# Optimization experiments

Hardware: AMD Instinct MI355X
Metric: run time of the kernel (lower is better)

## Reference

```python
import jax, jax.numpy as jnp
import numpy as np

N, E, D, G, L = 100_000, 500_000, 128, 512, 4
BN_EPS = 1e-5

def _bn(v, g, b):
    # BatchNorm1d in training mode: biased batch stats over node/graph axis
    m = v.mean(0)
    var = v.var(0)
    return (v - m) * jax.lax.rsqrt(var + BN_EPS) * g + b

def setup_inputs() -> dict:
    key = jax.random.key(0)
    ks = jax.random.split(key, 12)
    s = 0.05
    return {
        "x": jax.random.normal(ks[0], (N, D), jnp.float32),
        "edge_index": jax.random.randint(ks[1], (2, E), 0, N, jnp.int64),
        "batch": jnp.sort(jax.random.randint(ks[2], (N,), 0, G, jnp.int64)),
        "num_graphs": G,
        "W1": jax.random.normal(ks[3], (L, D, 2 * D), jnp.float32) * s,
        "b1": jnp.zeros((L, 2 * D), jnp.float32),
        "g1": jnp.ones((L, 2 * D), jnp.float32),
        "be1": jnp.zeros((L, 2 * D), jnp.float32),
        "W2": jax.random.normal(ks[4], (L, 2 * D, D), jnp.float32) * s,
        "b2": jnp.zeros((L, D), jnp.float32),
        "gbn": jnp.ones((L, D), jnp.float32),
        "bbn": jnp.zeros((L, D), jnp.float32),
        "eps": jnp.zeros((L,), jnp.float32),
        "cW1": jax.random.normal(ks[5], (3 * D, D), jnp.float32) * s,
        "cb1": jnp.zeros((D,), jnp.float32),
        "cg": jnp.ones((D,), jnp.float32),
        "cbeta": jnp.zeros((D,), jnp.float32),
        "cW2": jax.random.normal(ks[6], (D, D // 2), jnp.float32) * s,
        "cb2": jnp.zeros((D // 2,), jnp.float32),
        "cW3": jax.random.normal(ks[7], (D // 2, 2), jnp.float32) * s,
        "cb3": jnp.zeros((2,), jnp.float32),
    }

def reference(x, edge_index, batch, num_graphs, W1, b1, g1, be1, W2, b2, gbn, bbn, eps,
              cW1, cb1, cg, cbeta, cW2, cb2, cW3, cb3):
    n = x.shape[0]
    src, dst = edge_index[0], edge_index[1]
    for l in range(W1.shape[0]):
        # GINConv: mlp((1+eps)*x + sum_{j in N(i)} x_j)  (scatter-add to dst)
        agg = jax.ops.segment_sum(x[src], dst, num_segments=n)
        h = (1.0 + eps[l]) * x + agg
        h = jax.nn.relu(_bn(h @ W1[l] + b1[l], g1[l], be1[l]))
        h = h @ W2[l] + b2[l]
        x = jax.nn.relu(_bn(h, gbn[l], bbn[l]))  # outer BN + ReLU (dropout off: eval)
    # multi-pool readout: add / mean / max per graph
    s = jax.ops.segment_sum(x, batch, num_segments=num_graphs)
    cnt = jax.ops.segment_sum(jnp.ones((n,), x.dtype), batch, num_segments=num_graphs)
    mean = s / jnp.maximum(cnt, 1.0)[:, None]
    mx = jax.ops.segment_max(x, batch, num_segments=num_graphs)
    z = jnp.concatenate([s, mean, mx], axis=-1)  # [G, 3*D]
    z = jax.nn.relu(_bn(z @ cW1 + cb1, cg, cbeta))
    z = jax.nn.relu(z @ cW2 + cb2)
    return z @ cW3 + cb3
```

## Files before the change

### kernel.cpp

```cpp
#include <hip/hip_runtime.h>
#include <cstdint>
#include <cstddef>

#define NN 100000
#define EE 500000
#define DD 128
#define GG 512
#define LL 4
#define BN_EPS 1e-5f

typedef __attribute__((ext_vector_type(8))) short short8;
typedef __attribute__((ext_vector_type(8))) unsigned short ushort8v;
typedef __attribute__((ext_vector_type(4))) float f32x4;

static __device__ __forceinline__ unsigned short f2bf(float f) {
  union { float f; unsigned u; } v;
  v.f = f;
  unsigned r = v.u + 0x7fffu + ((v.u >> 16) & 1u);
  return (unsigned short)(r >> 16);
}
static __device__ __forceinline__ float bf2f(unsigned short u) {
  union { unsigned u; float f; } v;
  v.u = ((unsigned)u) << 16;
  return v.f;
}


__global__ void k_hist(const int* __restrict__ ei, int* __restrict__ cnt) {
  int e = blockIdx.x * 256 + threadIdx.x;
  if (e < EE) {
    int d = ei[EE + e];
    if (d >= 0 && d < NN) atomicAdd(&cnt[d], 1);
  }
}

__global__ void k_part(const int* __restrict__ cnt, int* __restrict__ part) {
  __shared__ int sm[1024];
  int t = threadIdx.x;
  int i = blockIdx.x * 1024 + t;
  sm[t] = (i < NN) ? cnt[i] : 0;
  __syncthreads();
  for (int off = 512; off > 0; off >>= 1) {
    if (t < off) sm[t] += sm[t + off];
    __syncthreads();
  }
  if (t == 0) part[blockIdx.x] = sm[0];
}

__global__ void k_scanpart(const int* __restrict__ part, int* __restrict__ partx, int nb) {
  __shared__ int sm[128];
  int t = threadIdx.x;
  int v = (t < nb) ? part[t] : 0;
  sm[t] = v;
  __syncthreads();
  for (int off = 1; off < 128; off <<= 1) {
    int u = (t >= off) ? sm[t - off] : 0;
    __syncthreads();
    sm[t] += u;
    __syncthreads();
  }
  if (t < nb) partx[t] = sm[t] - v;
}

__global__ void k_rs(const int* __restrict__ cnt, const int* __restrict__ partx,
                     int* __restrict__ rs, int* __restrict__ cur) {
  __shared__ int sm[1024];
  int t = threadIdx.x;
  int i = blockIdx.x * 1024 + t;
  int v = (i < NN) ? cnt[i] : 0;
  sm[t] = v;
  __syncthreads();
  for (int off = 1; off < 1024; off <<= 1) {
    int u = (t >= off) ? sm[t - off] : 0;
    __syncthreads();
    sm[t] += u;
    __syncthreads();
  }
  if (i < NN) {
    int excl = partx[blockIdx.x] + sm[t] - v;
    rs[i] = excl;
    cur[i] = excl;
    if (i == NN - 1) rs[NN] = excl + v;
  }
}

__global__ void k_fill(const int* __restrict__ ei, int* __restrict__ cur,
                       int* __restrict__ ci) {
  int e = blockIdx.x * 256 + threadIdx.x;
  if (e < EE) {
    int s = ei[e];
    int d = ei[EE + e];
    if (d >= 0 && d < NN && s >= 0 && s < NN) {
      int pos = atomicAdd(&cur[d], 1);
      if (pos >= 0 && pos < EE) ci[pos] = s;
    }
  }
}


__global__ void k_conv(const float* __restrict__ W1, const float* __restrict__ W2,
                       unsigned short* __restrict__ W1t, unsigned short* __restrict__ W2t) {
  int idx = blockIdx.x * 256 + threadIdx.x;
  if (idx < 4 * 256 * 128) {
    {
      int l = idx >> 15, rem = idx & 32767;
      int nc = rem >> 7, k = rem & 127;
      W1t[idx] = f2bf(W1[(l << 15) + k * 256 + nc]);
    }
    {
      int l = idx >> 15, rem = idx & 32767;
      int nc = rem >> 8, k = rem & 255;
      W2t[idx] = f2bf(W2[(l << 15) + k * 128 + nc]);
    }
  }
}


__global__ void k_x2bf(const float* __restrict__ x, unsigned short* __restrict__ xb) {
  int i = blockIdx.x * 256 + threadIdx.x;
  if (i < NN * DD / 4) {
    float4 v = *(const float4*)(x + (size_t)i * 4);
    ushort4 o;
    o.x = f2bf(v.x); o.y = f2bf(v.y); o.z = f2bf(v.z); o.w = f2bf(v.w);
    *(ushort4*)(xb + (size_t)i * 4) = o;
  }
}


__global__ __launch_bounds__(256) void k_agg_bf16(
    const unsigned short* __restrict__ X, const int* __restrict__ rs,
    const int* __restrict__ ci, const float* __restrict__ epsv, int l, int mode,
    const float* __restrict__ tsc, const float* __restrict__ tsh,
    unsigned short* __restrict__ h0, int n) {
  int idx = blockIdx.x * 256 + threadIdx.x;
  int node = idx >> 4;
  int c8 = (idx & 15) << 3;
  if (node >= n) return;
  float sa[8], sb[8];
  if (mode) {
    float4 a0 = *(const float4*)(tsc + c8), a1 = *(const float4*)(tsc + c8 + 4);
    float4 b0 = *(const float4*)(tsh + c8), b1 = *(const float4*)(tsh + c8 + 4);
    sa[0] = a0.x; sa[1] = a0.y; sa[2] = a0.z; sa[3] = a0.w;
    sa[4] = a1.x; sa[5] = a1.y; sa[6] = a1.z; sa[7] = a1.w;
    sb[0] = b0.x; sb[1] = b0.y; sb[2] = b0.z; sb[3] = b0.w;
    sb[4] = b1.x; sb[5] = b1.y; sb[6] = b1.z; sb[7] = b1.w;
  }
  float se = 1.f + epsv[l];
  ushort8v v = *(const ushort8v*)(X + (size_t)node * DD + c8);
  float acc[8];
#pragma unroll
  for (int j = 0; j < 8; ++j) {
    float f = bf2f(v[j]);
    if (mode) f = fmaxf(0.f, f * sa[j] + sb[j]);
    acc[j] = se * f;
  }
  int e0 = rs[node], e1 = rs[node + 1];
  ushort8v un;
  if (e0 < e1) un = *(const ushort8v*)(X + (size_t)ci[e0] * DD + c8);
  for (int e = e0; e < e1; ++e) {
    ushort8v uc = un;
    if (e + 1 < e1) un = *(const ushort8v*)(X + (size_t)ci[e + 1] * DD + c8);
#pragma unroll
    for (int j = 0; j < 8; ++j) {
      float f = bf2f(uc[j]);
      if (mode) f = fmaxf(0.f, f * sa[j] + sb[j]);
      acc[j] += f;
    }
  }
  ushort8v o;
#pragma unroll
  for (int j = 0; j < 8; ++j) o[j] = f2bf(acc[j]);
  *(ushort8v*)(h0 + (size_t)node * DD + c8) = o;
}


__global__ __launch_bounds__(512) void k_mom(
    const unsigned short* __restrict__ h0, float* __restrict__ M2s,
    float* __restrict__ css, int n) {
  constexpr int HT = 264;
  constexpr int NCH = (NN + 255) / 256;
  constexpr int NBLK = 196;
  __shared__ __align__(16) unsigned short Ht[128 * HT];
  __shared__ float lcs[128];
  int tid = threadIdx.x;
  int lane = tid & 63, wave = tid >> 6;
  int quad = lane >> 4, l15 = lane & 15;
  if (tid < 128) lcs[tid] = 0.f;
  int c8 = (tid & 15) << 3;
  int rloc = tid >> 4;
  float csr[8];
#pragma unroll
  for (int j = 0; j < 8; ++j) csr[j] = 0.f;
  f32x4 acc[8];
#pragma unroll
  for (int j = 0; j < 8; ++j) acc[j] = (f32x4){0.f, 0.f, 0.f, 0.f};

  for (int ch = blockIdx.x; ch < NCH; ch += NBLK) {
    int n0 = ch * 256;
    __syncthreads();
#pragma unroll
    for (int pass = 0; pass < 8; ++pass) {
      int nl = rloc + pass * 32;
      int gr = n0 + nl;
      ushort8v v = (ushort8v){0, 0, 0, 0, 0, 0, 0, 0};
      if (gr < n) v = *(const ushort8v*)(h0 + (size_t)gr * DD + c8);
#pragma unroll
      for (int j = 0; j < 8; ++j) {
        int row = c8 + j;
        int sb = (nl >> 3) ^ ((row >> 3) & 7);
        Ht[row * HT + (sb << 3) + (nl & 7)] = v[j];
        csr[j] += bf2f(v[j]);
      }
    }
    __syncthreads();
#pragma unroll
    for (int kc = 0; kc < 8; ++kc) {
      int b = kc * 4 + quad;
      int arow = wave * 16 + l15;
      short8 avv =
          *(const short8*)(&Ht[arow * HT + ((b ^ ((arow >> 3) & 7)) << 3)]);
#pragma unroll
      for (int j = 0; j < 8; ++j) {
        int brow = j * 16 + l15;
        short8 bvv =
            *(const short8*)(&Ht[brow * HT + ((b ^ ((brow >> 3) & 7)) << 3)]);
        acc[j] = __builtin_amdgcn_mfma_f32_16x16x32_bf16(avv, bvv, acc[j], 0, 0, 0);
      }
    }
  }
  float* M2 = M2s + (size_t)blockIdx.x * 16384;
  int lr = wave * 16 + quad * 4;
#pragma unroll
  for (int j = 0; j < 8; ++j)
#pragma unroll
    for (int g = 0; g < 4; ++g)
      M2[(lr + g) * 128 + j * 16 + l15] = acc[j][g];
#pragma unroll
  for (int j = 0; j < 8; ++j) atomicAdd(&lcs[c8 + j], csr[j]);
  __syncthreads();
  if (tid < 128) css[(size_t)blockIdx.x * 128 + tid] = lcs[tid];
}

__global__ void k_red(const float* __restrict__ M2s, const float* __restrict__ css,
                      float* __restrict__ M2f, float* __restrict__ csf) {
  int i = blockIdx.x * 256 + threadIdx.x;
  float s = 0.f;
  for (int k = 0; k < 196; ++k) s += M2s[(size_t)k * 16384 + i];
  M2f[i] = s;
  if (i < 128) {
    float c = 0.f;
    for (int k = 0; k < 196; ++k) c += css[(size_t)k * 128 + i];
    csf[i] = c;
  }
}

__global__ __launch_bounds__(128) void k_bn1(
    const float* __restrict__ M2, const float* __restrict__ cs,
    const unsigned short* __restrict__ W1t_l, const float* __restrict__ g1_l,
    const float* __restrict__ be1_l, float* __restrict__ osc,
    float* __restrict__ osh) {
  __shared__ float wsh[128];
  __shared__ float red1[2], red2[2];
  int c = blockIdx.x, t = threadIdx.x;
  float w = bf2f(W1t_l[c * 128 + t]);
  wsh[t] = w;
  __syncthreads();
  float inner = 0.f;
#pragma unroll 4
  for (int k = 0; k < 128; ++k) inner = fmaf(M2[t * 128 + k], wsh[k], inner);
  float s1 = w * inner;
  float s2 = w * cs[t];
#pragma unroll
  for (int off = 32; off > 0; off >>= 1) {
    s1 += __shfl_xor(s1, off, 64);
    s2 += __shfl_xor(s2, off, 64);
  }
  if ((t & 63) == 0) { red1[t >> 6] = s1; red2[t >> 6] = s2; }
  __syncthreads();
  if (t == 0) {
    float q = (red1[0] + red1[1]) * (1.0f / NN);
    float um = (red2[0] + red2[1]) * (1.0f / NN);
    float var = fmaxf(q - um * um, 0.f);
    float sc = g1_l[c] * rsqrtf(var + BN_EPS);
    osc[c] = sc;
    osh[c] = be1_l[c] - um * sc;
  }
}


__global__ __launch_bounds__(512, 4) void k_gfused(
    const unsigned short* __restrict__ A, const float* __restrict__ sc1,
    const float* __restrict__ sh1, const unsigned short* __restrict__ W1t_l,
    const unsigned short* __restrict__ W2t_l, const float* __restrict__ b2_l,
    unsigned short* __restrict__ C, float* __restrict__ psum,
    float* __restrict__ psq, int n) {
  constexpr int BST = 72;
  constexpr int HP = 136;
  __shared__ __align__(16) unsigned short Bsm[2][128 * BST];
  __shared__ __align__(16) unsigned short H[128 * HP];
  __shared__ float bsum[128], bsq[128];

  int tid = threadIdx.x;
  int lane = tid & 63, wave = tid >> 6;
  int quad = lane >> 4, l15 = lane & 15;
  int row0 = blockIdx.x * 128;
  int r = row0 + wave * 16 + l15;
  bool valid = r < n;

  short8 av[4];
#pragma unroll
  for (int ks = 0; ks < 4; ++ks) {
    av[ks] = (short8){0, 0, 0, 0, 0, 0, 0, 0};
    if (valid) av[ks] = *(const short8*)(A + (size_t)r * 128 + ks * 32 + quad * 8);
  }

  ushort8v pA[2], pB[2];
  f32x4 acc1[8], acc2[8];
#pragma unroll
  for (int j = 0; j < 8; ++j) acc1[j] = (f32x4){0.f, 0.f, 0.f, 0.f};
#pragma unroll
  for (int j = 0; j < 8; ++j) acc2[j] = (f32x4){0.f, 0.f, 0.f, 0.f};

#define LD_W1(dst, cg, kc)                                                      \
  {                                                                             \
    _Pragma("unroll") for (int it = 0; it < 2; ++it) {                          \
      int f = tid + it * 512, rr = f >> 3, cc = (f & 7) << 3;                   \
      dst[it] = *(const ushort8v*)(W1t_l + (size_t)((cg)*128 + rr) * 128 +      \
                                   (kc)*64 + cc);                               \
    }                                                                           \
  }
#define LD_W2(dst, kc2)                                                         \
  {                                                                             \
    _Pragma("unroll") for (int it = 0; it < 2; ++it) {                          \
      int f = tid + it * 512, rr = f >> 3, cc = (f & 7) << 3;                   \
      dst[it] = *(const ushort8v*)(W2t_l + (size_t)rr * 256 + (kc2)*64 + cc);   \
    }                                                                           \
  }
#define ST_B(buf, src)                                                          \
  {                                                                             \
    _Pragma("unroll") for (int it = 0; it < 2; ++it) {                          \
      int f = tid + it * 512, rr = f >> 3, cc = (f & 7) << 3;                   \
      *(ushort8v*)(&Bsm[buf][rr * BST + cc]) = src[it];                         \
    }                                                                           \
  }
#define MM1(buf, k2)                                                            \
  {                                                                             \
    _Pragma("unroll") for (int kk = 0; kk < 2; ++kk) {                          \
      int ko = kk * 32 + quad * 8;                                              \
      short8 a = av[(k2)*2 + kk];                                               \
      _Pragma("unroll") for (int cf = 0; cf < 8; ++cf) {                        \
        short8 bv = *(const short8*)(&Bsm[buf][(cf * 16 + l15) * BST + ko]);    \
        acc1[cf] = __builtin_amdgcn_mfma_f32_16x16x32_bf16(a, bv, acc1[cf],     \
                                                           0, 0, 0);            \
      }                                                                         \
    }                                                                           \
  }
#define MM2(buf, half)                                                          \
  {                                                                             \
    _Pragma("unroll") for (int kk = 0; kk < 64; kk += 32) {                     \
      int ko = kk + quad * 8;                                                   \
      short8 a = *(const short8*)(&H[(wave * 16 + l15) * HP + (half)*64 + ko]); \
      _Pragma("unroll") for (int cf = 0; cf < 8; ++cf) {                        \
        short8 bv = *(const short8*)(&Bsm[buf][(cf * 16 + l15) * BST + ko]);    \
        acc2[cf] = __builtin_amdgcn_mfma_f32_16x16x32_bf16(a, bv, acc2[cf],     \
                                                           0, 0, 0);            \
      }                                                                         \
    }                                                                           \
  }
#define EPI(cg)                                                                 \
  {                                                                             \
    int lrb = wave * 16 + quad * 4;                                             \
    _Pragma("unroll") for (int cf = 0; cf < 8; ++cf) {                          \
      int col = (cg)*128 + cf * 16 + l15;                                       \
      float sc = sc1[col], sh = sh1[col];                                       \
      _Pragma("unroll") for (int g = 0; g < 4; ++g)                             \
          H[(lrb + g) * HP + cf * 16 + l15] =                                   \
              f2bf(fmaxf(0.f, acc1[cf][g] * sc + sh));                          \
    }                                                                           \
  }
#define ZACC1                                                                   \
  {                                                                             \
    _Pragma("unroll") for (int j = 0; j < 8; ++j)                               \
        acc1[j] = (f32x4){0.f, 0.f, 0.f, 0.f};                                  \
  }

  LD_W1(pA, 0, 0)
  LD_W1(pB, 0, 1)
  ST_B(0, pA)
  __syncthreads();
  LD_W2(pA, 0) MM1(0, 0) ST_B(1, pB) __syncthreads();
  LD_W2(pB, 1) MM1(1, 1) EPI(0) ST_B(0, pA) __syncthreads();
  LD_W1(pA, 1, 0) MM2(0, 0) ST_B(1, pB) __syncthreads();
  LD_W1(pB, 1, 1) MM2(1, 1) ST_B(0, pA) __syncthreads();
  LD_W2(pA, 2) ZACC1 MM1(0, 0) ST_B(1, pB) __syncthreads();
  LD_W2(pB, 3) MM1(1, 1) EPI(1) ST_B(0, pA) __syncthreads();
  MM2(0, 0) ST_B(1, pB) __syncthreads();
  MM2(1, 1)

  __syncthreads();
  unsigned short* Ct = H;
  if (tid < 128) { bsum[tid] = 0.f; bsq[tid] = 0.f; }
  float s8[8], q8[8];
#pragma unroll
  for (int j = 0; j < 8; ++j) { s8[j] = 0.f; q8[j] = 0.f; }
  int lrbase = wave * 16 + quad * 4;
#pragma unroll
  for (int cf = 0; cf < 8; ++cf) {
    float bv = b2_l[cf * 16 + l15];
#pragma unroll
    for (int g = 0; g < 4; ++g) {
      int lr = lrbase + g;
      float e = acc2[cf][g] + bv;
      Ct[lr * HP + cf * 16 + l15] = f2bf(e);
      if (row0 + lr < n) { s8[cf] += e; q8[cf] += e * e; }
    }
  }
#pragma unroll
  for (int cf = 0; cf < 8; ++cf) {
    s8[cf] += __shfl_xor(s8[cf], 16, 64);
    s8[cf] += __shfl_xor(s8[cf], 32, 64);
    q8[cf] += __shfl_xor(q8[cf], 16, 64);
    q8[cf] += __shfl_xor(q8[cf], 32, 64);
  }
  __syncthreads();
  if (quad == 0) {
#pragma unroll
    for (int cf = 0; cf < 8; ++cf) {
      atomicAdd(&bsum[cf * 16 + l15], s8[cf]);
      atomicAdd(&bsq[cf * 16 + l15], q8[cf]);
    }
  }
#pragma unroll
  for (int it = 0; it < 4; ++it) {
    int f = tid + it * 512;
    int rr = f >> 4, cc = (f & 15) << 3;
    int gr = row0 + rr;
    if (gr < n)
      *(ushort8v*)(C + (size_t)gr * 128 + cc) = *(const ushort8v*)(&Ct[rr * HP + cc]);
  }
  __syncthreads();
  if (tid < 128) {
    psum[(size_t)blockIdx.x * 128 + tid] = bsum[tid];
    psq[(size_t)blockIdx.x * 128 + tid] = bsq[tid];
  }
#undef LD_W1
#undef LD_W2
#undef ST_B
#undef MM1
#undef MM2
#undef EPI
#undef ZACC1
}


__global__ __launch_bounds__(256) void k_finred(
    const float* __restrict__ psum, const float* __restrict__ psq, int nb, int nc,
    const float* __restrict__ g, const float* __restrict__ be,
    float* __restrict__ osc, float* __restrict__ osh, float invn) {
  __shared__ float ws[4], wq[4];
  int col = blockIdx.x;
  int t = threadIdx.x;
  float s = 0.f, q = 0.f;
  for (int b = t; b < nb; b += 256) {
    s += psum[(size_t)b * nc + col];
    q += psq[(size_t)b * nc + col];
  }
#pragma unroll
  for (int off = 32; off > 0; off >>= 1) {
    s += __shfl_xor(s, off, 64);
    q += __shfl_xor(q, off, 64);
  }
  if ((t & 63) == 0) { ws[t >> 6] = s; wq[t >> 6] = q; }
  __syncthreads();
  if (t == 0) {
    s = ws[0] + ws[1] + ws[2] + ws[3];
    q = wq[0] + wq[1] + wq[2] + wq[3];
    float m = s * invn;
    float v = fmaxf(q * invn - m * m, 0.f);
    float sc = g[col] * rsqrtf(v + BN_EPS);
    osc[col] = sc;
    osh[col] = be[col] - m * sc;
  }
}


__global__ __launch_bounds__(256) void k_statz(
    const float* __restrict__ z1, const float* __restrict__ g,
    const float* __restrict__ be, float* __restrict__ osc, float* __restrict__ osh) {
  __shared__ float ws[4], wq[4];
  int col = blockIdx.x;
  int t = threadIdx.x;
  float s = 0.f, q = 0.f;
  for (int b = t; b < GG; b += 256) {
    float v = z1[(size_t)b * 128 + col];
    s += v;
    q += v * v;
  }
#pragma unroll
  for (int off = 32; off > 0; off >>= 1) {
    s += __shfl_xor(s, off, 64);
    q += __shfl_xor(q, off, 64);
  }
  if ((t & 63) == 0) { ws[t >> 6] = s; wq[t >> 6] = q; }
  __syncthreads();
  if (t == 0) {
    s = ws[0] + ws[1] + ws[2] + ws[3];
    q = wq[0] + wq[1] + wq[2] + wq[3];
    float m = s / (float)GG;
    float v = fmaxf(q / (float)GG - m * m, 0.f);
    float sc = g[col] * rsqrtf(v + BN_EPS);
    osc[col] = sc;
    osh[col] = be[col] - m * sc;
  }
}


static __device__ __forceinline__ int lb_i32(const int* a, int n, int key) {
  int lo = 0, hi = n;
  while (lo < hi) {
    int mid = (lo + hi) >> 1;
    if (a[mid] < key) lo = mid + 1; else hi = mid;
  }
  return lo;
}

__global__ __launch_bounds__(512) void k_pool(
    const unsigned short* __restrict__ X, const int* __restrict__ batch,
    const float* __restrict__ tsc, const float* __restrict__ tsh,
    float* __restrict__ z, int n) {
  __shared__ int slo, shi;
  __shared__ float ssum[8][128], smax[8][128];
  int g = blockIdx.x;
  int t = threadIdx.x;
  int sg = t >> 6;
  int c2 = (t & 63) << 1;
  if (t == 0) {
    slo = lb_i32(batch, n, g);
    shi = lb_i32(batch, n, g + 1);
  }
  __syncthreads();
  int lo = slo, hi = shi;
  float a0 = tsc[c2], a1 = tsc[c2 + 1];
  float b0 = tsh[c2], b1 = tsh[c2 + 1];
  float s0 = 0.f, s1 = 0.f;
  float m0 = -3.402823466e38f, m1 = -3.402823466e38f;
  for (int i = lo + sg; i < hi; i += 8) {
    unsigned u = *(const unsigned*)(X + (size_t)i * DD + c2);
    float v0 = fmaxf(0.f, bf2f((unsigned short)(u & 0xffff)) * a0 + b0);
    float v1 = fmaxf(0.f, bf2f((unsigned short)(u >> 16)) * a1 + b1);
    s0 += v0; m0 = fmaxf(m0, v0);
    s1 += v1; m1 = fmaxf(m1, v1);
  }
  ssum[sg][c2] = s0; ssum[sg][c2 + 1] = s1;
  smax[sg][c2] = m0; smax[sg][c2 + 1] = m1;
  __syncthreads();
  if (t < 128) {
    float S = 0.f, M = -3.402823466e38f;
#pragma unroll
    for (int k = 0; k < 8; ++k) {
      S += ssum[k][t];
      M = fmaxf(M, smax[k][t]);
    }
    float cntf = (float)(hi - lo);
    z[(size_t)g * 384 + t] = S;
    z[(size_t)g * 384 + 128 + t] = S / fmaxf(cntf, 1.f);
    z[(size_t)g * 384 + 256 + t] = M;
  }
}


__global__ void k_cls1(const float* __restrict__ z, const float* __restrict__ cW1,
                       const float* __restrict__ cb1, float* __restrict__ z1) {
  __shared__ float zr[384];
  int g = blockIdx.x;
  int c = threadIdx.x;
  for (int i = c; i < 384; i += 128) zr[i] = z[(size_t)g * 384 + i];
  __syncthreads();
  float s = cb1[c];
#pragma unroll 4
  for (int k = 0; k < 384; ++k) s = fmaf(zr[k], cW1[(size_t)k * 128 + c], s);
  z1[(size_t)g * 128 + c] = s;
}

__global__ void k_cls2(const float* __restrict__ z1, const float* __restrict__ csc,
                       const float* __restrict__ csh, const float* __restrict__ cW2,
                       const float* __restrict__ cb2, const float* __restrict__ cW3,
                       const float* __restrict__ cb3, float* __restrict__ out) {
  __shared__ float z1n[128];
  __shared__ float z2s[64];
  int g = blockIdx.x;
  int t = threadIdx.x;
  z1n[t] = fmaxf(0.f, z1[(size_t)g * 128 + t] * csc[t] + csh[t]);
  __syncthreads();
  if (t < 64) {
    float s = cb2[t];
#pragma unroll 4
    for (int k = 0; k < 128; ++k) s = fmaf(z1n[k], cW2[(size_t)k * 64 + t], s);
    z2s[t] = fmaxf(0.f, s);
  }
  __syncthreads();
  if (t < 2) {
    float s = cb3[t];
#pragma unroll 4
    for (int c = 0; c < 64; ++c) s = fmaf(z2s[c], cW3[(size_t)c * 2 + t], s);
    out[(size_t)g * 2 + t] = s;
  }
}


extern "C" void kernel_launch(void* const* d_in, const int* in_sizes, int n_in,
                              void* d_out, int out_size, void* d_ws, size_t ws_size,
                              hipStream_t stream) {
  const float* x = (const float*)d_in[0];
  const int* ei = (const int*)d_in[1];
  const int* batch = (const int*)d_in[2];
  const float* W1 = (const float*)d_in[4];
  const float* b1 = (const float*)d_in[5];
  const float* g1 = (const float*)d_in[6];
  const float* be1 = (const float*)d_in[7];
  const float* W2 = (const float*)d_in[8];
  const float* b2 = (const float*)d_in[9];
  const float* gbn = (const float*)d_in[10];
  const float* bbn = (const float*)d_in[11];
  const float* epsv = (const float*)d_in[12];
  const float* cW1 = (const float*)d_in[13];
  const float* cb1 = (const float*)d_in[14];
  const float* cg = (const float*)d_in[15];
  const float* cbeta = (const float*)d_in[16];
  const float* cW2 = (const float*)d_in[17];
  const float* cb2 = (const float*)d_in[18];
  const float* cW3 = (const float*)d_in[19];
  const float* cb3 = (const float*)d_in[20];
  float* out = (float*)d_out;
  (void)b1;

  char* p = (char*)d_ws;
  auto alloc = [&](size_t bytes) {
    char* r = p;
    p += (bytes + 255) & ~(size_t)255;
    return r;
  };
  const int NB = (NN + 127) / 128;
  int* cnt = (int*)alloc((size_t)NN * 4);
  int* rs = (int*)alloc((size_t)(NN + 1) * 4);
  int* cur = (int*)alloc((size_t)NN * 4);
  int* ci = (int*)alloc((size_t)EE * 4);
  int* part = (int*)alloc(128 * 4);
  int* partx = (int*)alloc(128 * 4);
  unsigned short* xbf = (unsigned short*)alloc((size_t)NN * DD * 2);
  unsigned short* h0 = (unsigned short*)alloc((size_t)NN * DD * 2);
  unsigned short* xp = (unsigned short*)alloc((size_t)NN * DD * 2);
  float* psum = (float*)alloc((size_t)NB * 128 * 4);
  float* psq = (float*)alloc((size_t)NB * 128 * 4);
  float* tsc1 = (float*)alloc(256 * 4);
  float* tsh1 = (float*)alloc(256 * 4);
  float* tscX = (float*)alloc(128 * 4);
  float* tshX = (float*)alloc(128 * 4);
  float* zbuf = (float*)alloc((size_t)GG * 384 * 4);
  float* z1 = (float*)alloc((size_t)GG * 128 * 4);
  unsigned short* W1t = (unsigned short*)alloc((size_t)4 * 256 * 128 * 2);
  unsigned short* W2t = (unsigned short*)alloc((size_t)4 * 128 * 256 * 2);
  float* M2s = (float*)alloc((size_t)196 * 16384 * 4);
  float* css = (float*)alloc((size_t)196 * 128 * 4);
  float* M2f = (float*)alloc((size_t)128 * 128 * 4);
  float* csf = (float*)alloc(128 * 4);
  (void)ws_size; (void)n_in; (void)in_sizes; (void)out_size;

  k_conv<<<512, 256, 0, stream>>>(W1, W2, W1t, W2t);
  k_x2bf<<<(NN * DD / 4 + 255) / 256, 256, 0, stream>>>(x, xbf);

  hipMemsetAsync(cnt, 0, (size_t)NN * 4, stream);
  k_hist<<<(EE + 255) / 256, 256, 0, stream>>>(ei, cnt);
  const int nscan = (NN + 1023) / 1024;
  k_part<<<nscan, 1024, 0, stream>>>(cnt, part);
  k_scanpart<<<1, 128, 0, stream>>>(part, partx, nscan);
  k_rs<<<nscan, 1024, 0, stream>>>(cnt, partx, rs, cur);
  k_fill<<<(EE + 255) / 256, 256, 0, stream>>>(ei, cur, ci);

  for (int l = 0; l < LL; ++l) {
    const unsigned short* Xl = (l == 0) ? xbf : xp;
    k_agg_bf16<<<(NN * 16 + 255) / 256, 256, 0, stream>>>(
        Xl, rs, ci, epsv, l, (l > 0) ? 1 : 0, tscX, tshX, h0, NN);
    k_mom<<<196, 512, 0, stream>>>(h0, M2s, css, NN);
    k_red<<<64, 256, 0, stream>>>(M2s, css, M2f, csf);
    k_bn1<<<256, 128, 0, stream>>>(M2f, csf, W1t + (size_t)l * 256 * 128,
                                   g1 + (size_t)l * 256, be1 + (size_t)l * 256,
                                   tsc1, tsh1);
    k_gfused<<<NB, 512, 0, stream>>>(
        h0, tsc1, tsh1, W1t + (size_t)l * 256 * 128, W2t + (size_t)l * 128 * 256,
        b2 + (size_t)l * 128, xp, psum, psq, NN);
    k_finred<<<128, 256, 0, stream>>>(psum, psq, NB, 128, gbn + (size_t)l * 128,
                                      bbn + (size_t)l * 128, tscX, tshX, 1.0f / NN);
  }

  k_pool<<<GG, 512, 0, stream>>>(xp, batch, tscX, tshX, zbuf, NN);
  k_cls1<<<GG, 128, 0, stream>>>(zbuf, cW1, cb1, z1);
  k_statz<<<128, 256, 0, stream>>>(z1, cg, cbeta, tscX, tshX);
  k_cls2<<<GG, 128, 0, stream>>>(z1, tscX, tshX, cW2, cb2, cW3, cb3, out);
}
```

Measured before the change: 754.8 us.

## Double rows per block in fused GIN MLP and unroll neighbor gather by four

The fused MLP kernel now handles 256 rows per block, with each wave computing two 16-row MFMA tiles. This reuses every weight tile loaded into shared memory across twice as many rows and halves the number of blocks. The cost is more registers and LDS per block, so the occupancy hint drops to 2 blocks per CU. Separately, the aggregation gather keeps four neighbor loads in flight instead of one, to hide memory latency on the irregular reads.

```diff
diff --git a/kernel.cpp b/kernel.cpp
--- a/kernel.cpp
+++ b/kernel.cpp
@@ -155,18 +155,34 @@
     acc[j] = se * f;
   }
   int e0 = rs[node], e1 = rs[node + 1];
-  ushort8v un;
-  if (e0 < e1) un = *(const ushort8v*)(X + (size_t)ci[e0] * DD + c8);
-  for (int e = e0; e < e1; ++e) {
-    ushort8v uc = un;
-    if (e + 1 < e1) un = *(const ushort8v*)(X + (size_t)ci[e + 1] * DD + c8);
-#pragma unroll
-    for (int j = 0; j < 8; ++j) {
-      float f = bf2f(uc[j]);
-      if (mode) f = fmaxf(0.f, f * sa[j] + sb[j]);
-      acc[j] += f;
-    }
-  }
+#define NLD(ee) (*(const ushort8v*)(X + (size_t)ci[ee] * DD + c8))
+#define NACC(uc)                                                  \
+  {                                                               \
+    _Pragma("unroll") for (int j = 0; j < 8; ++j) {               \
+      float f = bf2f(uc[j]);                                      \
+      if (mode) f = fmaxf(0.f, f * sa[j] + sb[j]);                \
+      acc[j] += f;                                                \
+    }                                                             \
+  }
+  ushort8v p0 = (ushort8v){0, 0, 0, 0, 0, 0, 0, 0};
+  ushort8v p1 = p0, p2 = p0, p3 = p0;
+  if (e0 + 0 < e1) p0 = NLD(e0 + 0);
+  if (e0 + 1 < e1) p1 = NLD(e0 + 1);
+  if (e0 + 2 < e1) p2 = NLD(e0 + 2);
+  if (e0 + 3 < e1) p3 = NLD(e0 + 3);
+  for (int e = e0; e < e1; e += 4) {
+    ushort8v c0 = p0, c1 = p1, c2 = p2, c3 = p3;
+    if (e + 4 < e1) p0 = NLD(e + 4);
+    if (e + 5 < e1) p1 = NLD(e + 5);
+    if (e + 6 < e1) p2 = NLD(e + 6);
+    if (e + 7 < e1) p3 = NLD(e + 7);
+    NACC(c0);
+    if (e + 1 < e1) NACC(c1);
+    if (e + 2 < e1) NACC(c2);
+    if (e + 3 < e1) NACC(c3);
+  }
+#undef NLD
+#undef NACC
   ushort8v o;
 #pragma unroll
   for (int j = 0; j < 8; ++j) o[j] = f2bf(acc[j]);
@@ -288,7 +304,7 @@
 }
 
 
-__global__ __launch_bounds__(512, 4) void k_gfused(
+__global__ __launch_bounds__(512, 2) void k_gfused(
     const unsigned short* __restrict__ A, const float* __restrict__ sc1,
     const float* __restrict__ sh1, const unsigned short* __restrict__ W1t_l,
     const unsigned short* __restrict__ W2t_l, const float* __restrict__ b2_l,
@@ -297,29 +313,34 @@
   constexpr int BST = 72;
   constexpr int HP = 136;
   __shared__ __align__(16) unsigned short Bsm[2][128 * BST];
-  __shared__ __align__(16) unsigned short H[128 * HP];
+  __shared__ __align__(16) unsigned short H[256 * HP];
   __shared__ float bsum[128], bsq[128];
 
   int tid = threadIdx.x;
   int lane = tid & 63, wave = tid >> 6;
   int quad = lane >> 4, l15 = lane & 15;
-  int row0 = blockIdx.x * 128;
-  int r = row0 + wave * 16 + l15;
-  bool valid = r < n;
-
-  short8 av[4];
+  int row0 = blockIdx.x * 256;
+  int r0 = row0 + wave * 32 + l15;
+  int r1 = r0 + 16;
+
+  short8 av0[4], av1[4];
 #pragma unroll
   for (int ks = 0; ks < 4; ++ks) {
-    av[ks] = (short8){0, 0, 0, 0, 0, 0, 0, 0};
-    if (valid) av[ks] = *(const short8*)(A + (size_t)r * 128 + ks * 32 + quad * 8);
+    av0[ks] = (short8){0, 0, 0, 0, 0, 0, 0, 0};
+    av1[ks] = (short8){0, 0, 0, 0, 0, 0, 0, 0};
+    if (r0 < n) av0[ks] = *(const short8*)(A + (size_t)r0 * 128 + ks * 32 + quad * 8);
+    if (r1 < n) av1[ks] = *(const short8*)(A + (size_t)r1 * 128 + ks * 32 + quad * 8);
   }
 
   ushort8v pA[2], pB[2];
-  f32x4 acc1[8], acc2[8];
-#pragma unroll
-  for (int j = 0; j < 8; ++j) acc1[j] = (f32x4){0.f, 0.f, 0.f, 0.f};
-#pragma unroll
-  for (int j = 0; j < 8; ++j) acc2[j] = (f32x4){0.f, 0.f, 0.f, 0.f};
+  f32x4 acc1a[8], acc1b[8], acc2a[8], acc2b[8];
+#pragma unroll
+  for (int j = 0; j < 8; ++j) {
+    acc1a[j] = (f32x4){0.f, 0.f, 0.f, 0.f};
+    acc1b[j] = (f32x4){0.f, 0.f, 0.f, 0.f};
+    acc2a[j] = (f32x4){0.f, 0.f, 0.f, 0.f};
+    acc2b[j] = (f32x4){0.f, 0.f, 0.f, 0.f};
+  }
 
 #define LD_W1(dst, cg, kc)                                                      \
   {                                                                             \
@@ -347,11 +368,14 @@
   {                                                                             \
     _Pragma("unroll") for (int kk = 0; kk < 2; ++kk) {                          \
       int ko = kk * 32 + quad * 8;                                              \
-      short8 a = av[(k2)*2 + kk];                                               \
+      short8 a0 = av0[(k2)*2 + kk];                                             \
+      short8 a1 = av1[(k2)*2 + kk];                                             \
       _Pragma("unroll") for (int cf = 0; cf < 8; ++cf) {                        \
         short8 bv = *(const short8*)(&Bsm[buf][(cf * 16 + l15) * BST + ko]);    \
-        acc1[cf] = __builtin_amdgcn_mfma_f32_16x16x32_bf16(a, bv, acc1[cf],     \
-                                                           0, 0, 0);            \
+        acc1a[cf] = __builtin_amdgcn_mfma_f32_16x16x32_bf16(a0, bv, acc1a[cf],  \
+                                                            0, 0, 0);           \
+        acc1b[cf] = __builtin_amdgcn_mfma_f32_16x16x32_bf16(a1, bv, acc1b[cf],  \
+                                                            0, 0, 0);           \
       }                                                                         \
     }                                                                           \
   }
@@ -359,29 +383,39 @@
   {                                                                             \
     _Pragma("unroll") for (int kk = 0; kk < 64; kk += 32) {                     \
       int ko = kk + quad * 8;                                                   \
-      short8 a = *(const short8*)(&H[(wave * 16 + l15) * HP + (half)*64 + ko]); \
+      short8 a0 =                                                               \
+          *(const short8*)(&H[(wave * 32 + l15) * HP + (half)*64 + ko]);        \
+      short8 a1 =                                                               \
+          *(const short8*)(&H[(wave * 32 + 16 + l15) * HP + (half)*64 + ko]);   \
       _Pragma("unroll") for (int cf = 0; cf < 8; ++cf) {                        \
         short8 bv = *(const short8*)(&Bsm[buf][(cf * 16 + l15) * BST + ko]);    \
-        acc2[cf] = __builtin_amdgcn_mfma_f32_16x16x32_bf16(a, bv, acc2[cf],     \
-                                                           0, 0, 0);            \
+        acc2a[cf] = __builtin_amdgcn_mfma_f32_16x16x32_bf16(a0, bv, acc2a[cf],  \
+                                                            0, 0, 0);           \
+        acc2b[cf] = __builtin_amdgcn_mfma_f32_16x16x32_bf16(a1, bv, acc2b[cf],  \
+                                                            0, 0, 0);           \
       }                                                                         \
     }                                                                           \
   }
 #define EPI(cg)                                                                 \
   {                                                                             \
-    int lrb = wave * 16 + quad * 4;                                             \
+    int lrb = wave * 32 + quad * 4;                                             \
     _Pragma("unroll") for (int cf = 0; cf < 8; ++cf) {                          \
       int col = (cg)*128 + cf * 16 + l15;                                       \
       float sc = sc1[col], sh = sh1[col];                                       \
-      _Pragma("unroll") for (int g = 0; g < 4; ++g)                             \
-          H[(lrb + g) * HP + cf * 16 + l15] =                                   \
-              f2bf(fmaxf(0.f, acc1[cf][g] * sc + sh));                          \
+      _Pragma("unroll") for (int g = 0; g < 4; ++g) {                           \
+        H[(lrb + g) * HP + cf * 16 + l15] =                                     \
+            f2bf(fmaxf(0.f, acc1a[cf][g] * sc + sh));                           \
+        H[(lrb + 16 + g) * HP + cf * 16 + l15] =                                \
+            f2bf(fmaxf(0.f, acc1b[cf][g] * sc + sh));                           \
+      }                                                                         \
     }                                                                           \
   }
 #define ZACC1                                                                   \
   {                                                                             \
-    _Pragma("unroll") for (int j = 0; j < 8; ++j)                               \
-        acc1[j] = (f32x4){0.f, 0.f, 0.f, 0.f};                                  \
+    _Pragma("unroll") for (int j = 0; j < 8; ++j) {                             \
+      acc1a[j] = (f32x4){0.f, 0.f, 0.f, 0.f};                                   \
+      acc1b[j] = (f32x4){0.f, 0.f, 0.f, 0.f};                                   \
+    }                                                                           \
   }
 
   LD_W1(pA, 0, 0)
@@ -403,16 +437,24 @@
   float s8[8], q8[8];
 #pragma unroll
   for (int j = 0; j < 8; ++j) { s8[j] = 0.f; q8[j] = 0.f; }
-  int lrbase = wave * 16 + quad * 4;
+  int lrbase = wave * 32 + quad * 4;
 #pragma unroll
   for (int cf = 0; cf < 8; ++cf) {
     float bv = b2_l[cf * 16 + l15];
 #pragma unroll
     for (int g = 0; g < 4; ++g) {
-      int lr = lrbase + g;
-      float e = acc2[cf][g] + bv;
-      Ct[lr * HP + cf * 16 + l15] = f2bf(e);
-      if (row0 + lr < n) { s8[cf] += e; q8[cf] += e * e; }
+      {
+        int lr = lrbase + g;
+        float e = acc2a[cf][g] + bv;
+        Ct[lr * HP + cf * 16 + l15] = f2bf(e);
+        if (row0 + lr < n) { s8[cf] += e; q8[cf] += e * e; }
+      }
+      {
+        int lr = lrbase + 16 + g;
+        float e = acc2b[cf][g] + bv;
+        Ct[lr * HP + cf * 16 + l15] = f2bf(e);
+        if (row0 + lr < n) { s8[cf] += e; q8[cf] += e * e; }
+      }
     }
   }
 #pragma unroll
@@ -431,7 +473,7 @@
     }
   }
 #pragma unroll
-  for (int it = 0; it < 4; ++it) {
+  for (int it = 0; it < 8; ++it) {
     int f = tid + it * 512;
     int rr = f >> 4, cc = (f & 15) << 3;
     int gr = row0 + rr;
@@ -640,7 +682,7 @@
     p += (bytes + 255) & ~(size_t)255;
     return r;
   };
-  const int NB = (NN + 127) / 128;
+  const int NB2 = (NN + 255) / 256;
   int* cnt = (int*)alloc((size_t)NN * 4);
   int* rs = (int*)alloc((size_t)(NN + 1) * 4);
   int* cur = (int*)alloc((size_t)NN * 4);
@@ -650,8 +692,8 @@
   unsigned short* xbf = (unsigned short*)alloc((size_t)NN * DD * 2);
   unsigned short* h0 = (unsigned short*)alloc((size_t)NN * DD * 2);
   unsigned short* xp = (unsigned short*)alloc((size_t)NN * DD * 2);
-  float* psum = (float*)alloc((size_t)NB * 128 * 4);
-  float* psq = (float*)alloc((size_t)NB * 128 * 4);
+  float* psum = (float*)alloc((size_t)NB2 * 128 * 4);
+  float* psq = (float*)alloc((size_t)NB2 * 128 * 4);
   float* tsc1 = (float*)alloc(256 * 4);
   float* tsh1 = (float*)alloc(256 * 4);
   float* tscX = (float*)alloc(128 * 4);
@@ -686,10 +728,10 @@
     k_bn1<<<256, 128, 0, stream>>>(M2f, csf, W1t + (size_t)l * 256 * 128,
                                    g1 + (size_t)l * 256, be1 + (size_t)l * 256,
                                    tsc1, tsh1);
-    k_gfused<<<NB, 512, 0, stream>>>(
+    k_gfused<<<NB2, 512, 0, stream>>>(
         h0, tsc1, tsh1, W1t + (size_t)l * 256 * 128, W2t + (size_t)l * 128 * 256,
         b2 + (size_t)l * 128, xp, psum, psq, NN);
-    k_finred<<<128, 256, 0, stream>>>(psum, psq, NB, 128, gbn + (size_t)l * 128,
+    k_finred<<<128, 256, 0, stream>>>(psum, psq, NB2, 128, gbn + (size_t)l * 128,
                                       bbn + (size_t)l * 128, tscX, tshX, 1.0f / NN);
   }
 
```

After: 713.1 us. 1.06x faster.
